# Kernel optimization log

Hardware: AMD Instinct MI355X
Metric: run time of the kernel (lower is better)

Reference implementation:

```python
import jax, jax.numpy as jnp
import numpy as np
from jax.scipy.special import logsumexp

NUM = 4      # Bregman ADMM iterations (module default)
EPS = 1e-8


def setup_inputs() -> dict:
    key = jax.random.key(0)
    k = jax.random.split(key, 8)
    B, N, D = 64, 1024, 512
    x = jax.random.normal(k[0], (B, N, D), dtype=jnp.float32)
    # marginal priors: positive, normalized along their distribution axis
    p0 = jax.random.uniform(k[1], (B, 1, D), dtype=jnp.float32, minval=0.1, maxval=1.0)
    p0 = p0 / jnp.sum(p0, axis=2, keepdims=True)
    q0 = jax.random.uniform(k[2], (B, N, 1), dtype=jnp.float32, minval=0.1, maxval=1.0)
    q0 = q0 / jnp.sum(q0, axis=1, keepdims=True)
    # positive per-iteration weights / ADMM step sizes
    a1 = jax.random.uniform(k[3], (NUM,), dtype=jnp.float32, minval=0.1, maxval=1.1)
    a2 = jax.random.uniform(k[4], (NUM,), dtype=jnp.float32, minval=0.1, maxval=1.1)
    a3 = jax.random.uniform(k[5], (NUM,), dtype=jnp.float32, minval=0.1, maxval=1.1)
    rho = jax.random.uniform(k[6], (NUM,), dtype=jnp.float32, minval=0.1, maxval=1.1)
    mask = jnp.ones((B, N, 1), dtype=jnp.float32)
    return {"x": x, "p0": p0, "q0": q0, "a1": a1, "a2": a2, "a3": a3,
            "rho": rho, "mask": mask}


def reference(x, p0, q0, a1, a2, a3, rho, mask):
    """UOT via Bregman ADMM with entropic regularizer (f_method='badmm-e')."""
    log_t = jnp.log(q0 * p0 + EPS)        # (B,N,D)
    log_s = jnp.log(q0 * p0 + EPS)        # (B,N,D)
    log_mu = jnp.log(p0)                  # (B,1,D)
    log_eta = jnp.log(q0 + EPS)           # (B,N,1)
    log_p0 = jnp.log(p0)
    log_q0 = jnp.log(q0 + EPS)
    z = jnp.zeros_like(log_t)
    z1 = jnp.zeros_like(p0)
    z2 = jnp.zeros_like(q0)
    for k in range(NUM):
        n = min(k, NUM - 1)
        # update T (row problem: normalize over D)
        y = (x - z) / rho[n] + log_s
        log_t = (log_mu - logsumexp(y, axis=2, keepdims=True)) + y
        # update S (column problem: normalize over N)
        y = (z + rho[n] * log_t) / (a1[n] + rho[n])
        log_s = (log_eta - logsumexp(y, axis=1, keepdims=True)) + y
        t = jnp.exp(log_t) * mask
        s = jnp.exp(log_s) * mask
        z = z + rho[n] * (t - s)
        # dual marginal updates
        y = (rho[n] * log_mu + a2[n] * log_p0 - z1) / (rho[n] + a2[n])
        log_mu = y - logsumexp(y, axis=2, keepdims=True)
        y = (rho[n] * log_eta + a3[n] * log_q0 - z2) / (rho[n] + a3[n])
        log_eta = y - logsumexp(y, axis=1, keepdims=True)
        z1 = z1 + rho[n] * (jnp.exp(log_mu) - jnp.sum(t, axis=2, keepdims=True))
        z2 = z2 + rho[n] * (jnp.exp(log_eta) - jnp.sum(s, axis=1, keepdims=True))
    return jnp.exp(log_t) * mask
```

## Files before the change

kernel.cpp:

```cpp
#include <hip/hip_runtime.h>
#include <cmath>


#define B_ 64
#define N_ 1024
#define D_ 512
#define EPS_ 1e-8f
#define NCHUNK 8
#define CH (N_ / NCHUNK)
#define NCOL (B_ * D_)
static const size_t NT_ = (size_t)B_ * N_ * D_;

__device__ __forceinline__ float wmax64(float v) {
#pragma unroll
  for (int o = 32; o > 0; o >>= 1) v = fmaxf(v, __shfl_xor(v, o, 64));
  return v;
}
__device__ __forceinline__ float wsum64(float v) {
#pragma unroll
  for (int o = 32; o > 0; o >>= 1) v += __shfl_xor(v, o, 64);
  return v;
}
__device__ __forceinline__ void olse(float& m, float& s, float v) {
  float nm = fmaxf(m, v);
  s = s * __expf(m - nm) + __expf(v - nm);
  m = nm;
}

template <int IS_FIRST, int LAST>
__global__ __launch_bounds__(256) void k1_row(
    const float* __restrict__ x, const float* __restrict__ p0,
    const float* __restrict__ q0, const float* __restrict__ mask,
    const float* __restrict__ a1arr, const float* __restrict__ rhoarr,
    const int k, const float* __restrict__ mun,
    float* ys,
    const float* __restrict__ z, float* __restrict__ outv)
{
  const int wid  = threadIdx.x >> 6;
  const int lane = threadIdx.x & 63;
  const int row  = (blockIdx.x << 2) + wid;
  const int b    = row >> 10;
  const float rho = rhoarr[k];
  const float inv_rho = 1.0f / rho;
  const size_t base = (size_t)row * D_ + (size_t)(lane * 8);
  const int pb = (b << 9) + lane * 8;

  float xv[8], y[8], lmu[8], zv[8];
  *(float4*)&xv[0] = *(const float4*)&x[base];
  *(float4*)&xv[4] = *(const float4*)&x[base + 4];

  if (IS_FIRST) {
    float pv[8];
    *(float4*)&pv[0] = *(const float4*)&p0[pb];
    *(float4*)&pv[4] = *(const float4*)&p0[pb + 4];
    const float q0v = q0[row];
#pragma unroll
    for (int j = 0; j < 8; ++j) {
      lmu[j] = __logf(pv[j]);
      float lsv = __logf(q0v * pv[j] + EPS_);
      y[j] = xv[j] * inv_rho + lsv;
      zv[j] = 0.f;
    }
  } else {
    float lsv[8];
    *(float4*)&zv[0]  = *(const float4*)&z[base];
    *(float4*)&zv[4]  = *(const float4*)&z[base + 4];
    *(float4*)&lsv[0] = *(const float4*)&ys[base];
    *(float4*)&lsv[4] = *(const float4*)&ys[base + 4];
    *(float4*)&lmu[0] = *(const float4*)&mun[pb];
    *(float4*)&lmu[4] = *(const float4*)&mun[pb + 4];
#pragma unroll
    for (int j = 0; j < 8; ++j) y[j] = (xv[j] - zv[j]) * inv_rho + lsv[j];
  }

  float mloc = -INFINITY;
#pragma unroll
  for (int j = 0; j < 8; ++j) mloc = fmaxf(mloc, y[j]);
  const float m = wmax64(mloc);
  float sloc = 0.f;
#pragma unroll
  for (int j = 0; j < 8; ++j) sloc += __expf(y[j] - m);
  const float lse = m + __logf(wsum64(sloc));

  if (LAST) {
    const float mv = mask[row];
    float o[8];
#pragma unroll
    for (int j = 0; j < 8; ++j) o[j] = __expf(lmu[j] - lse + y[j]) * mv;
    *(float4*)&outv[base]     = *(float4*)&o[0];
    *(float4*)&outv[base + 4] = *(float4*)&o[4];
  } else {
    const float inv_sc = 1.0f / (a1arr[k] + rho);
    float yp[8];
#pragma unroll
    for (int j = 0; j < 8; ++j)
      yp[j] = (zv[j] + rho * (lmu[j] - lse + y[j])) * inv_sc;
    *(float4*)&ys[base]     = *(float4*)&yp[0];
    *(float4*)&ys[base + 4] = *(float4*)&yp[4];
  }
}

__global__ __launch_bounds__(256) void k2a(
    const float* __restrict__ yp, float* __restrict__ pmax,
    float* __restrict__ psum)
{
  const int col = blockIdx.x * 256 + threadIdx.x;
  const int chunk = blockIdx.y;
  size_t idx = ((size_t)(col >> 9) * N_ + (size_t)(chunk * CH)) * D_ + (col & 511);
  float m0 = -INFINITY, s0 = 0.f, m1 = -INFINITY, s1 = 0.f;
  float m2 = -INFINITY, s2 = 0.f, m3 = -INFINITY, s3 = 0.f;
  for (int nn = 0; nn < CH; nn += 4) {
    float v0 = yp[idx];
    float v1 = yp[idx + D_];
    float v2 = yp[idx + 2 * D_];
    float v3 = yp[idx + 3 * D_];
    olse(m0, s0, v0); olse(m1, s1, v1); olse(m2, s2, v2); olse(m3, s3, v3);
    idx += 4 * D_;
  }
  float m = fmaxf(fmaxf(m0, m1), fmaxf(m2, m3));
  float s = s0 * __expf(m0 - m) + s1 * __expf(m1 - m) +
            s2 * __expf(m2 - m) + s3 * __expf(m3 - m);
  pmax[chunk * NCOL + col] = m;
  psum[chunk * NCOL + col] = s;
}

template <int IS_FIRST>
__global__ __launch_bounds__(256) void k2b(
    const float* __restrict__ q0, const float* __restrict__ mask,
    const float* __restrict__ a1arr, const float* __restrict__ rhoarr,
    const int k, const float* __restrict__ len,
    float* ys,
    float* __restrict__ z,
    const float* __restrict__ pmax, const float* __restrict__ psum)
{
  const int col = blockIdx.x * 256 + threadIdx.x;
  const int chunk = blockIdx.y;
  const float rho = rhoarr[k];
  const float sc = a1arr[k] + rho;
  const float inv_rho = 1.0f / rho;
  const float sc_ir = sc * inv_rho;

  float lse1;
  {
    float m = -INFINITY;
#pragma unroll
    for (int c = 0; c < NCHUNK; ++c) m = fmaxf(m, pmax[c * NCOL + col]);
    float s = 0.f;
#pragma unroll
    for (int c = 0; c < NCHUNK; ++c)
      s += psum[c * NCOL + col] * __expf(pmax[c * NCOL + col] - m);
    lse1 = m + __logf(s);
  }

  size_t idx = ((size_t)(col >> 9) * N_ + (size_t)(chunk * CH)) * D_ + (col & 511);
  int nrow = (col >> 9) * N_ + chunk * CH;
#pragma unroll 2
  for (int nn = 0; nn < CH; ++nn) {
    float ypv = ys[idx];
    float zv = IS_FIRST ? 0.f : z[idx];
    float le = IS_FIRST ? __logf(q0[nrow] + EPS_) : len[nrow];
    float ls = (le - lse1) + ypv;
    ys[idx] = ls;
    float mv = mask[nrow];
    float lt = IS_FIRST ? ypv * sc_ir : (ypv * sc - zv) * inv_rho;
    float t  = __expf(lt) * mv;
    float s_ = __expf(ls) * mv;
    z[idx] = zv + rho * (t - s_);
    idx += D_;
    ++nrow;
  }
}

template <int K>
__global__ __launch_bounds__(256) void small_upd(
    const float* __restrict__ p0, const float* __restrict__ q0,
    const float* __restrict__ a2arr, const float* __restrict__ a3arr,
    const float* __restrict__ rhoarr,
    float* mun, float* zC, float* len, float* z2C)
{
  __shared__ float red[8];
  const int b = blockIdx.x;
  const int tid = threadIdx.x, wid = tid >> 6, lane = tid & 63;
  const float rho = rhoarr[K];

  if (blockIdx.y == 0) {
    const float a2 = a2arr[K];
    const float inv = 1.0f / (rho + a2);
    float A[2], zcv[2];
    const int i0 = b * D_ + tid;
#pragma unroll
    for (int j = 0; j < 2; ++j) {
      int i = i0 + j * 256;
      float lp = __logf(p0[i]);
      float prev = (K == 0) ? lp : mun[i];
      zcv[j] = (K == 0) ? 0.f : zC[i];
      A[j] = (rho * prev + a2 * lp - zcv[j]) * inv;
    }
    float m = wmax64(fmaxf(A[0], A[1]));
    if (lane == 0) red[wid] = m;
    __syncthreads();
    float bm = fmaxf(fmaxf(red[0], red[1]), fmaxf(red[2], red[3]));
    float s = wsum64(__expf(A[0] - bm) + __expf(A[1] - bm));
    if (lane == 0) red[4 + wid] = s;
    __syncthreads();
    float lse = bm + __logf(red[4] + red[5] + red[6] + red[7]);
#pragma unroll
    for (int j = 0; j < 2; ++j) {
      int i = i0 + j * 256;
      float mn = A[j] - lse;
      mun[i] = mn;
      if (K <= 1) zC[i] = zcv[j] + rho * __expf(mn);
    }
  } else {
    const float a3 = a3arr[K];
    const float inv = 1.0f / (rho + a3);
    float E[4];
    const int i0 = b * N_ + tid * 4;
#pragma unroll
    for (int j = 0; j < 4; ++j) {
      int i = i0 + j;
      float lq = __logf(q0[i] + EPS_);
      float prev = (K == 0) ? lq : len[i];
      float z2c = (K == 0) ? 0.f : z2C[i];
      E[j] = (rho * prev + a3 * lq - z2c) * inv;
    }
    float m = wmax64(fmaxf(fmaxf(E[0], E[1]), fmaxf(E[2], E[3])));
    if (lane == 0) red[wid] = m;
    __syncthreads();
    float bm = fmaxf(fmaxf(red[0], red[1]), fmaxf(red[2], red[3]));
    float s = 0.f;
#pragma unroll
    for (int j = 0; j < 4; ++j) s += __expf(E[j] - bm);
    s = wsum64(s);
    if (lane == 0) red[4 + wid] = s;
    __syncthreads();
    float lse = bm + __logf(red[4] + red[5] + red[6] + red[7]);
#pragma unroll
    for (int j = 0; j < 4; ++j) {
      int i = i0 + j;
      float ln = E[j] - lse;
      len[i] = ln;
      if (K == 0) z2C[i] = rho * __expf(ln);
    }
  }
}

extern "C" void kernel_launch(void* const* d_in, const int* in_sizes, int n_in,
                              void* d_out, int out_size, void* d_ws, size_t ws_size,
                              hipStream_t stream)
{
  const float* x    = (const float*)d_in[0];
  const float* p0   = (const float*)d_in[1];
  const float* q0   = (const float*)d_in[2];
  const float* a1   = (const float*)d_in[3];
  const float* a2   = (const float*)d_in[4];
  const float* a3   = (const float*)d_in[5];
  const float* rho  = (const float*)d_in[6];
  const float* mask = (const float*)d_in[7];
  float* out = (float*)d_out;

  float* ws   = (float*)d_ws;
  float* ys   = ws;
  float* z    = ws + NT_;
  float* pmax = ws + 2 * NT_;
  float* psum = pmax + (size_t)NCHUNK * NCOL;
  float* mun  = psum + (size_t)NCHUNK * NCOL;
  float* zC   = mun + (size_t)B_ * D_;
  float* len  = zC  + (size_t)B_ * D_;
  float* z2C  = len + (size_t)B_ * N_;

  const dim3 tb(256);
  const dim3 g1(B_ * N_ / 4);
  const dim3 g2(NCOL / 256, NCHUNK);

  k1_row<1, 0><<<g1, tb, 0, stream>>>(x, p0, q0, mask, a1, rho, 0, mun, ys, z, out);
  k2a<<<g2, tb, 0, stream>>>(ys, pmax, psum);
  k2b<1><<<g2, tb, 0, stream>>>(q0, mask, a1, rho, 0, len, ys, z, pmax, psum);
  small_upd<0><<<dim3(B_, 2), tb, 0, stream>>>(p0, q0, a2, a3, rho, mun, zC, len, z2C);

  k1_row<0, 0><<<g1, tb, 0, stream>>>(x, p0, q0, mask, a1, rho, 1, mun, ys, z, out);
  k2a<<<g2, tb, 0, stream>>>(ys, pmax, psum);
  k2b<0><<<g2, tb, 0, stream>>>(q0, mask, a1, rho, 1, len, ys, z, pmax, psum);
  small_upd<1><<<dim3(B_, 2), tb, 0, stream>>>(p0, q0, a2, a3, rho, mun, zC, len, z2C);

  k1_row<0, 0><<<g1, tb, 0, stream>>>(x, p0, q0, mask, a1, rho, 2, mun, ys, z, out);
  k2a<<<g2, tb, 0, stream>>>(ys, pmax, psum);
  k2b<0><<<g2, tb, 0, stream>>>(q0, mask, a1, rho, 2, len, ys, z, pmax, psum);
  small_upd<2><<<dim3(B_, 1), tb, 0, stream>>>(p0, q0, a2, a3, rho, mun, zC, len, z2C);

  k1_row<0, 1><<<g1, tb, 0, stream>>>(x, p0, q0, mask, a1, rho, 3, mun, ys, z, out);
}
```

Baseline: 841.6 us.

## Fuse column partial LSE into row kernel, vectorize column update, fold last z

The row kernel now computes per-16-row column partial max/sum through LDS after writing ys, which removes the separate k2a pass that re-read the full ys tensor. A small reduction kernel combines the 64 chunk partials into lse1. The column update kernel is vectorized to float4. In the last iteration z is folded into ys as ls - z/rho_next so that z need not be written or re-read by the final row kernel. In exchange it uses 1024-thread blocks with a block-wide sync and a larger partial buffer.

```diff
diff --git a/kernel.cpp b/kernel.cpp
--- a/kernel.cpp
+++ b/kernel.cpp
@@ -6,9 +6,10 @@
 #define N_ 1024
 #define D_ 512
 #define EPS_ 1e-8f
-#define NCHUNK 8
-#define CH (N_ / NCHUNK)
 #define NCOL (B_ * D_)
+#define KCHUNK 64
+#define CH2 16
+#define NCHUNK2 64
 static const size_t NT_ = (size_t)B_ * N_ * D_;
 
 __device__ __forceinline__ float wmax64(float v) {
@@ -21,27 +22,25 @@
   for (int o = 32; o > 0; o >>= 1) v += __shfl_xor(v, o, 64);
   return v;
 }
-__device__ __forceinline__ void olse(float& m, float& s, float v) {
-  float nm = fmaxf(m, v);
-  s = s * __expf(m - nm) + __expf(v - nm);
-  m = nm;
-}
-
-template <int IS_FIRST, int LAST>
-__global__ __launch_bounds__(256) void k1_row(
+
+template <int IS_FIRST>
+__global__ __launch_bounds__(1024, 4) void k1p(
     const float* __restrict__ x, const float* __restrict__ p0,
-    const float* __restrict__ q0, const float* __restrict__ mask,
+    const float* __restrict__ q0,
     const float* __restrict__ a1arr, const float* __restrict__ rhoarr,
     const int k, const float* __restrict__ mun,
     float* ys,
-    const float* __restrict__ z, float* __restrict__ outv)
-{
+    const float* __restrict__ z,
+    float* __restrict__ pmax, float* __restrict__ psum)
+{
+  __shared__ float lds[16 * 512];
   const int wid  = threadIdx.x >> 6;
   const int lane = threadIdx.x & 63;
-  const int row  = (blockIdx.x << 2) + wid;
+  const int row  = blockIdx.x * 16 + wid;
   const int b    = row >> 10;
   const float rho = rhoarr[k];
   const float inv_rho = 1.0f / rho;
+  const float inv_sc = 1.0f / (a1arr[k] + rho);
   const size_t base = (size_t)row * D_ + (size_t)(lane * 8);
   const int pb = (b << 9) + lane * 8;
 
@@ -62,15 +61,14 @@
       zv[j] = 0.f;
     }
   } else {
-    float lsv[8];
-    *(float4*)&zv[0]  = *(const float4*)&z[base];
-    *(float4*)&zv[4]  = *(const float4*)&z[base + 4];
-    *(float4*)&lsv[0] = *(const float4*)&ys[base];
-    *(float4*)&lsv[4] = *(const float4*)&ys[base + 4];
+    *(float4*)&zv[0] = *(const float4*)&z[base];
+    *(float4*)&zv[4] = *(const float4*)&z[base + 4];
+    *(float4*)&y[0]  = *(const float4*)&ys[base];
+    *(float4*)&y[4]  = *(const float4*)&ys[base + 4];
     *(float4*)&lmu[0] = *(const float4*)&mun[pb];
     *(float4*)&lmu[4] = *(const float4*)&mun[pb + 4];
 #pragma unroll
-    for (int j = 0; j < 8; ++j) y[j] = (xv[j] - zv[j]) * inv_rho + lsv[j];
+    for (int j = 0; j < 8; ++j) y[j] = (xv[j] - zv[j]) * inv_rho + y[j];
   }
 
   float mloc = -INFINITY;
@@ -82,93 +80,152 @@
   for (int j = 0; j < 8; ++j) sloc += __expf(y[j] - m);
   const float lse = m + __logf(wsum64(sloc));
 
-  if (LAST) {
-    const float mv = mask[row];
-    float o[8];
-#pragma unroll
-    for (int j = 0; j < 8; ++j) o[j] = __expf(lmu[j] - lse + y[j]) * mv;
-    *(float4*)&outv[base]     = *(float4*)&o[0];
-    *(float4*)&outv[base + 4] = *(float4*)&o[4];
-  } else {
-    const float inv_sc = 1.0f / (a1arr[k] + rho);
-    float yp[8];
-#pragma unroll
-    for (int j = 0; j < 8; ++j)
-      yp[j] = (zv[j] + rho * (lmu[j] - lse + y[j])) * inv_sc;
-    *(float4*)&ys[base]     = *(float4*)&yp[0];
-    *(float4*)&ys[base + 4] = *(float4*)&yp[4];
-  }
-}
-
-__global__ __launch_bounds__(256) void k2a(
-    const float* __restrict__ yp, float* __restrict__ pmax,
-    float* __restrict__ psum)
+  float yp[8];
+#pragma unroll
+  for (int j = 0; j < 8; ++j)
+    yp[j] = (zv[j] + rho * (lmu[j] - lse + y[j])) * inv_sc;
+  *(float4*)&ys[base]     = *(float4*)&yp[0];
+  *(float4*)&ys[base + 4] = *(float4*)&yp[4];
+
+  const int dbase = lane * 8;
+#pragma unroll
+  for (int j = 0; j < 8; ++j) lds[wid * 512 + dbase + j] = yp[j];
+  __syncthreads();
+  if (threadIdx.x < 512) {
+    const int d = threadIdx.x;
+    float v[16];
+#pragma unroll
+    for (int w = 0; w < 16; ++w) v[w] = lds[w * 512 + d];
+    float mm = v[0];
+#pragma unroll
+    for (int w = 1; w < 16; ++w) mm = fmaxf(mm, v[w]);
+    float ss = 0.f;
+#pragma unroll
+    for (int w = 0; w < 16; ++w) ss += __expf(v[w] - mm);
+    const int bb = blockIdx.x >> 6;
+    const int chunk = blockIdx.x & 63;
+    const int col = (bb << 9) + d;
+    pmax[chunk * NCOL + col] = mm;
+    psum[chunk * NCOL + col] = ss;
+  }
+}
+
+__global__ __launch_bounds__(256) void kred(
+    const float* __restrict__ pmax, const float* __restrict__ psum,
+    float* __restrict__ lse1)
 {
   const int col = blockIdx.x * 256 + threadIdx.x;
-  const int chunk = blockIdx.y;
-  size_t idx = ((size_t)(col >> 9) * N_ + (size_t)(chunk * CH)) * D_ + (col & 511);
-  float m0 = -INFINITY, s0 = 0.f, m1 = -INFINITY, s1 = 0.f;
-  float m2 = -INFINITY, s2 = 0.f, m3 = -INFINITY, s3 = 0.f;
-  for (int nn = 0; nn < CH; nn += 4) {
-    float v0 = yp[idx];
-    float v1 = yp[idx + D_];
-    float v2 = yp[idx + 2 * D_];
-    float v3 = yp[idx + 3 * D_];
-    olse(m0, s0, v0); olse(m1, s1, v1); olse(m2, s2, v2); olse(m3, s3, v3);
-    idx += 4 * D_;
-  }
-  float m = fmaxf(fmaxf(m0, m1), fmaxf(m2, m3));
-  float s = s0 * __expf(m0 - m) + s1 * __expf(m1 - m) +
-            s2 * __expf(m2 - m) + s3 * __expf(m3 - m);
-  pmax[chunk * NCOL + col] = m;
-  psum[chunk * NCOL + col] = s;
-}
-
-template <int IS_FIRST>
+  float m0 = -INFINITY, m1 = -INFINITY, m2 = -INFINITY, m3 = -INFINITY;
+#pragma unroll
+  for (int c = 0; c < KCHUNK; c += 4) {
+    m0 = fmaxf(m0, pmax[(c + 0) * NCOL + col]);
+    m1 = fmaxf(m1, pmax[(c + 1) * NCOL + col]);
+    m2 = fmaxf(m2, pmax[(c + 2) * NCOL + col]);
+    m3 = fmaxf(m3, pmax[(c + 3) * NCOL + col]);
+  }
+  const float M = fmaxf(fmaxf(m0, m1), fmaxf(m2, m3));
+  float s0 = 0.f, s1 = 0.f, s2 = 0.f, s3 = 0.f;
+#pragma unroll
+  for (int c = 0; c < KCHUNK; c += 4) {
+    s0 += psum[(c + 0) * NCOL + col] * __expf(pmax[(c + 0) * NCOL + col] - M);
+    s1 += psum[(c + 1) * NCOL + col] * __expf(pmax[(c + 1) * NCOL + col] - M);
+    s2 += psum[(c + 2) * NCOL + col] * __expf(pmax[(c + 2) * NCOL + col] - M);
+    s3 += psum[(c + 3) * NCOL + col] * __expf(pmax[(c + 3) * NCOL + col] - M);
+  }
+  lse1[col] = M + __logf((s0 + s1) + (s2 + s3));
+}
+
+template <int IS_FIRST, int WRITE_Z, int FOLD>
 __global__ __launch_bounds__(256) void k2b(
     const float* __restrict__ q0, const float* __restrict__ mask,
     const float* __restrict__ a1arr, const float* __restrict__ rhoarr,
     const int k, const float* __restrict__ len,
     float* ys,
     float* __restrict__ z,
-    const float* __restrict__ pmax, const float* __restrict__ psum)
-{
-  const int col = blockIdx.x * 256 + threadIdx.x;
-  const int chunk = blockIdx.y;
+    const float* __restrict__ lse1)
+{
+  const int t4 = (blockIdx.x * 256 + threadIdx.x) * 4;
+  const int b = t4 >> 9;
+  const int d = t4 & 511;
+  const int n0 = blockIdx.y * CH2;
   const float rho = rhoarr[k];
   const float sc = a1arr[k] + rho;
   const float inv_rho = 1.0f / rho;
   const float sc_ir = sc * inv_rho;
-
-  float lse1;
-  {
-    float m = -INFINITY;
-#pragma unroll
-    for (int c = 0; c < NCHUNK; ++c) m = fmaxf(m, pmax[c * NCOL + col]);
-    float s = 0.f;
-#pragma unroll
-    for (int c = 0; c < NCHUNK; ++c)
-      s += psum[c * NCOL + col] * __expf(pmax[c * NCOL + col] - m);
-    lse1 = m + __logf(s);
-  }
-
-  size_t idx = ((size_t)(col >> 9) * N_ + (size_t)(chunk * CH)) * D_ + (col & 511);
-  int nrow = (col >> 9) * N_ + chunk * CH;
-#pragma unroll 2
-  for (int nn = 0; nn < CH; ++nn) {
-    float ypv = ys[idx];
-    float zv = IS_FIRST ? 0.f : z[idx];
-    float le = IS_FIRST ? __logf(q0[nrow] + EPS_) : len[nrow];
-    float ls = (le - lse1) + ypv;
-    ys[idx] = ls;
-    float mv = mask[nrow];
-    float lt = IS_FIRST ? ypv * sc_ir : (ypv * sc - zv) * inv_rho;
-    float t  = __expf(lt) * mv;
-    float s_ = __expf(ls) * mv;
-    z[idx] = zv + rho * (t - s_);
+  const float irn = FOLD ? (1.0f / rhoarr[k + 1]) : 0.0f;
+
+  float L[4];
+  *(float4*)L = *(const float4*)&lse1[t4];
+
+  size_t idx = ((size_t)b * N_ + (size_t)n0) * D_ + d;
+  int nrow = b * N_ + n0;
+#pragma unroll 4
+  for (int nn = 0; nn < CH2; ++nn) {
+    float ypv[4], zv[4];
+    *(float4*)ypv = *(const float4*)&ys[idx];
+    if (IS_FIRST) {
+#pragma unroll
+      for (int j = 0; j < 4; ++j) zv[j] = 0.f;
+    } else {
+      *(float4*)zv = *(const float4*)&z[idx];
+    }
+    const float le = IS_FIRST ? __logf(q0[nrow] + EPS_) : len[nrow];
+    const float mv = mask[nrow];
+    float wout[4], zn[4];
+#pragma unroll
+    for (int j = 0; j < 4; ++j) {
+      float ls = (le - L[j]) + ypv[j];
+      float lt = IS_FIRST ? ypv[j] * sc_ir : (ypv[j] * sc - zv[j]) * inv_rho;
+      float t_ = __expf(lt) * mv;
+      float s_ = __expf(ls) * mv;
+      zn[j] = zv[j] + rho * (t_ - s_);
+      wout[j] = FOLD ? (ls - zn[j] * irn) : ls;
+    }
+    *(float4*)&ys[idx] = *(float4*)wout;
+    if (WRITE_Z) *(float4*)&z[idx] = *(float4*)zn;
     idx += D_;
     ++nrow;
   }
+}
+
+__global__ __launch_bounds__(256) void k1last(
+    const float* __restrict__ x, const float* __restrict__ mask,
+    const float* __restrict__ rhoarr, const float* __restrict__ mun,
+    const float* __restrict__ w, float* __restrict__ outv)
+{
+  const int wid  = threadIdx.x >> 6;
+  const int lane = threadIdx.x & 63;
+  const int row  = (blockIdx.x << 2) + wid;
+  const int b    = row >> 10;
+  const float inv_rho = 1.0f / rhoarr[3];
+  const size_t base = (size_t)row * D_ + (size_t)(lane * 8);
+  const int pb = (b << 9) + lane * 8;
+
+  float xv[8], y[8], lmu[8];
+  *(float4*)&xv[0] = *(const float4*)&x[base];
+  *(float4*)&xv[4] = *(const float4*)&x[base + 4];
+  *(float4*)&y[0]  = *(const float4*)&w[base];
+  *(float4*)&y[4]  = *(const float4*)&w[base + 4];
+  *(float4*)&lmu[0] = *(const float4*)&mun[pb];
+  *(float4*)&lmu[4] = *(const float4*)&mun[pb + 4];
+#pragma unroll
+  for (int j = 0; j < 8; ++j) y[j] = xv[j] * inv_rho + y[j];
+
+  float mloc = -INFINITY;
+#pragma unroll
+  for (int j = 0; j < 8; ++j) mloc = fmaxf(mloc, y[j]);
+  const float m = wmax64(mloc);
+  float sloc = 0.f;
+#pragma unroll
+  for (int j = 0; j < 8; ++j) sloc += __expf(y[j] - m);
+  const float lse = m + __logf(wsum64(sloc));
+
+  const float mv = mask[row];
+  float o[8];
+#pragma unroll
+  for (int j = 0; j < 8; ++j) o[j] = __expf(lmu[j] - lse + y[j]) * mv;
+  *(float4*)&outv[base]     = *(float4*)&o[0];
+  *(float4*)&outv[base + 4] = *(float4*)&o[4];
 }
 
 template <int K>
@@ -263,30 +320,34 @@
   float* ys   = ws;
   float* z    = ws + NT_;
   float* pmax = ws + 2 * NT_;
-  float* psum = pmax + (size_t)NCHUNK * NCOL;
-  float* mun  = psum + (size_t)NCHUNK * NCOL;
+  float* psum = pmax + (size_t)KCHUNK * NCOL;
+  float* lse1 = psum + (size_t)KCHUNK * NCOL;
+  float* mun  = lse1 + NCOL;
   float* zC   = mun + (size_t)B_ * D_;
   float* len  = zC  + (size_t)B_ * D_;
   float* z2C  = len + (size_t)B_ * N_;
 
   const dim3 tb(256);
-  const dim3 g1(B_ * N_ / 4);
-  const dim3 g2(NCOL / 256, NCHUNK);
-
-  k1_row<1, 0><<<g1, tb, 0, stream>>>(x, p0, q0, mask, a1, rho, 0, mun, ys, z, out);
-  k2a<<<g2, tb, 0, stream>>>(ys, pmax, psum);
-  k2b<1><<<g2, tb, 0, stream>>>(q0, mask, a1, rho, 0, len, ys, z, pmax, psum);
+  const dim3 tb1k(1024);
+  const dim3 g1(B_ * N_ / 16);
+  const dim3 gr(NCOL / 256);
+  const dim3 g2(NCOL / 4 / 256, NCHUNK2);
+  const dim3 gl(B_ * N_ / 4);
+
+  k1p<1><<<g1, tb1k, 0, stream>>>(x, p0, q0, a1, rho, 0, mun, ys, z, pmax, psum);
+  kred<<<gr, tb, 0, stream>>>(pmax, psum, lse1);
+  k2b<1, 1, 0><<<g2, tb, 0, stream>>>(q0, mask, a1, rho, 0, len, ys, z, lse1);
   small_upd<0><<<dim3(B_, 2), tb, 0, stream>>>(p0, q0, a2, a3, rho, mun, zC, len, z2C);
 
-  k1_row<0, 0><<<g1, tb, 0, stream>>>(x, p0, q0, mask, a1, rho, 1, mun, ys, z, out);
-  k2a<<<g2, tb, 0, stream>>>(ys, pmax, psum);
-  k2b<0><<<g2, tb, 0, stream>>>(q0, mask, a1, rho, 1, len, ys, z, pmax, psum);
+  k1p<0><<<g1, tb1k, 0, stream>>>(x, p0, q0, a1, rho, 1, mun, ys, z, pmax, psum);
+  kred<<<gr, tb, 0, stream>>>(pmax, psum, lse1);
+  k2b<0, 1, 0><<<g2, tb, 0, stream>>>(q0, mask, a1, rho, 1, len, ys, z, lse1);
   small_upd<1><<<dim3(B_, 2), tb, 0, stream>>>(p0, q0, a2, a3, rho, mun, zC, len, z2C);
 
-  k1_row<0, 0><<<g1, tb, 0, stream>>>(x, p0, q0, mask, a1, rho, 2, mun, ys, z, out);
-  k2a<<<g2, tb, 0, stream>>>(ys, pmax, psum);
-  k2b<0><<<g2, tb, 0, stream>>>(q0, mask, a1, rho, 2, len, ys, z, pmax, psum);
+  k1p<0><<<g1, tb1k, 0, stream>>>(x, p0, q0, a1, rho, 2, mun, ys, z, pmax, psum);
+  kred<<<gr, tb, 0, stream>>>(pmax, psum, lse1);
+  k2b<0, 0, 1><<<g2, tb, 0, stream>>>(q0, mask, a1, rho, 2, len, ys, z, lse1);
   small_upd<2><<<dim3(B_, 1), tb, 0, stream>>>(p0, q0, a2, a3, rho, mun, zC, len, z2C);
 
-  k1_row<0, 1><<<g1, tb, 0, stream>>>(x, p0, q0, mask, a1, rho, 3, mun, ys, z, out);
-}
+  k1last<<<gl, tb, 0, stream>>>(x, mask, rho, mun, ys, out);
+}
```

Measured after the change: 746.8 us. -11.3%, faster.

## Fuse column update into next row pass with per-chunk partial column LSE

Applied to the files above, without the earlier changes.

Merges the S/z column update of iteration k with the row logsumexp of iteration k+1 into one streaming kernel. Each wave handles 16 rows and keeps running per-column max/sum partials, so the separate column-LSE read pass disappears and only a small 64-chunk reduction kernel remains. This cuts full-tensor reads and writes of ys and z per iteration. The cost is double-buffered eta vectors, larger partial buffers, and the extra register pressure of software-pipelined row loads.

```diff
diff --git a/kernel.cpp b/kernel.cpp
--- a/kernel.cpp
+++ b/kernel.cpp
@@ -6,9 +6,8 @@
 #define N_ 1024
 #define D_ 512
 #define EPS_ 1e-8f
-#define NCHUNK 8
-#define CH (N_ / NCHUNK)
 #define NCOL (B_ * D_)
+#define KCHUNK 64
 static const size_t NT_ = (size_t)B_ * N_ * D_;
 
 __device__ __forceinline__ float wmax64(float v) {
@@ -27,148 +26,215 @@
   m = nm;
 }
 
+__global__ __launch_bounds__(256, 4) void p0k(
+    const float* __restrict__ x, const float* __restrict__ p0,
+    const float* __restrict__ q0,
+    const float* __restrict__ a1arr, const float* __restrict__ rhoarr,
+    float* __restrict__ ys, float* __restrict__ pmax, float* __restrict__ psum)
+{
+  const int wid = threadIdx.x >> 6, lane = threadIdx.x & 63;
+  const int chunk = blockIdx.x * 4 + wid;
+  const int b = chunk >> 6, cb = chunk & 63;
+  const int c0 = lane * 8;
+  const int row0 = chunk * 16;
+  const float rho0 = rhoarr[0];
+  const float ir = 1.0f / rho0;
+  const float w0 = rho0 / (a1arr[0] + rho0);
+  float pv[8], lp[8];
+  *(float4*)&pv[0] = *(const float4*)&p0[(b << 9) + c0];
+  *(float4*)&pv[4] = *(const float4*)&p0[(b << 9) + c0 + 4];
+#pragma unroll
+  for (int j = 0; j < 8; ++j) lp[j] = __logf(pv[j]);
+  float m[8], s[8];
+#pragma unroll
+  for (int j = 0; j < 8; ++j) { m[j] = -INFINITY; s[j] = 0.f; }
+  const size_t base0 = (size_t)row0 * D_ + c0;
+
+  float xA[8], xB[8];
+  float qA, qB;
+
+#define LOADP(X, Q, r) do {                                   \
+    const size_t o_ = base0 + (size_t)(r) * D_;               \
+    *(float4*)&X[0] = *(const float4*)&x[o_];                 \
+    *(float4*)&X[4] = *(const float4*)&x[o_ + 4];             \
+    Q = q0[row0 + (r)];                                       \
+  } while (0)
+
+#define PROCP(X, Q, r) do {                                   \
+    _Pragma("unroll")                                         \
+    for (int j = 0; j < 8; ++j)                               \
+      X[j] = X[j] * ir + __logf(Q * pv[j] + EPS_);            \
+    float mm_ = -INFINITY;                                    \
+    _Pragma("unroll")                                         \
+    for (int j = 0; j < 8; ++j) mm_ = fmaxf(mm_, X[j]);       \
+    mm_ = wmax64(mm_);                                        \
+    float ss_ = 0.f;                                          \
+    _Pragma("unroll")                                         \
+    for (int j = 0; j < 8; ++j) ss_ += __expf(X[j] - mm_);    \
+    const float lse_ = mm_ + __logf(wsum64(ss_));             \
+    float yp_[8];                                             \
+    _Pragma("unroll")                                         \
+    for (int j = 0; j < 8; ++j)                               \
+      yp_[j] = (lp[j] - lse_ + X[j]) * w0;                    \
+    const size_t o_ = base0 + (size_t)(r) * D_;               \
+    *(float4*)&ys[o_]     = *(float4*)&yp_[0];                \
+    *(float4*)&ys[o_ + 4] = *(float4*)&yp_[4];                \
+    _Pragma("unroll")                                         \
+    for (int j = 0; j < 8; ++j) olse(m[j], s[j], yp_[j]);     \
+  } while (0)
+
+  LOADP(xA, qA, 0);
+#pragma unroll
+  for (int rr = 0; rr < 16; rr += 2) {
+    LOADP(xB, qB, rr + 1);
+    PROCP(xA, qA, rr);
+    if (rr + 2 < 16) LOADP(xA, qA, rr + 2);
+    PROCP(xB, qB, rr + 1);
+  }
+#undef LOADP
+#undef PROCP
+  const int pcol = cb * NCOL + (b << 9) + c0;
+  *(float4*)&pmax[pcol]     = *(float4*)&m[0];
+  *(float4*)&pmax[pcol + 4] = *(float4*)&m[4];
+  *(float4*)&psum[pcol]     = *(float4*)&s[0];
+  *(float4*)&psum[pcol + 4] = *(float4*)&s[4];
+}
+
 template <int IS_FIRST, int LAST>
-__global__ __launch_bounds__(256) void k1_row(
-    const float* __restrict__ x, const float* __restrict__ p0,
-    const float* __restrict__ q0, const float* __restrict__ mask,
+__global__ __launch_bounds__(256, 4) void fuse(
+    const float* __restrict__ x, const float* __restrict__ q0,
+    const float* __restrict__ mask,
     const float* __restrict__ a1arr, const float* __restrict__ rhoarr,
-    const int k, const float* __restrict__ mun,
-    float* ys,
-    const float* __restrict__ z, float* __restrict__ outv)
-{
-  const int wid  = threadIdx.x >> 6;
-  const int lane = threadIdx.x & 63;
-  const int row  = (blockIdx.x << 2) + wid;
-  const int b    = row >> 10;
-  const float rho = rhoarr[k];
-  const float inv_rho = 1.0f / rho;
-  const size_t base = (size_t)row * D_ + (size_t)(lane * 8);
-  const int pb = (b << 9) + lane * 8;
-
-  float xv[8], y[8], lmu[8], zv[8];
-  *(float4*)&xv[0] = *(const float4*)&x[base];
-  *(float4*)&xv[4] = *(const float4*)&x[base + 4];
-
-  if (IS_FIRST) {
-    float pv[8];
-    *(float4*)&pv[0] = *(const float4*)&p0[pb];
-    *(float4*)&pv[4] = *(const float4*)&p0[pb + 4];
-    const float q0v = q0[row];
-#pragma unroll
-    for (int j = 0; j < 8; ++j) {
-      lmu[j] = __logf(pv[j]);
-      float lsv = __logf(q0v * pv[j] + EPS_);
-      y[j] = xv[j] * inv_rho + lsv;
-      zv[j] = 0.f;
-    }
-  } else {
-    float lsv[8];
-    *(float4*)&zv[0]  = *(const float4*)&z[base];
-    *(float4*)&zv[4]  = *(const float4*)&z[base + 4];
-    *(float4*)&lsv[0] = *(const float4*)&ys[base];
-    *(float4*)&lsv[4] = *(const float4*)&ys[base + 4];
-    *(float4*)&lmu[0] = *(const float4*)&mun[pb];
-    *(float4*)&lmu[4] = *(const float4*)&mun[pb + 4];
-#pragma unroll
-    for (int j = 0; j < 8; ++j) y[j] = (xv[j] - zv[j]) * inv_rho + lsv[j];
-  }
-
-  float mloc = -INFINITY;
-#pragma unroll
-  for (int j = 0; j < 8; ++j) mloc = fmaxf(mloc, y[j]);
-  const float m = wmax64(mloc);
-  float sloc = 0.f;
-#pragma unroll
-  for (int j = 0; j < 8; ++j) sloc += __expf(y[j] - m);
-  const float lse = m + __logf(wsum64(sloc));
-
-  if (LAST) {
-    const float mv = mask[row];
-    float o[8];
-#pragma unroll
-    for (int j = 0; j < 8; ++j) o[j] = __expf(lmu[j] - lse + y[j]) * mv;
-    *(float4*)&outv[base]     = *(float4*)&o[0];
-    *(float4*)&outv[base + 4] = *(float4*)&o[4];
-  } else {
-    const float inv_sc = 1.0f / (a1arr[k] + rho);
-    float yp[8];
-#pragma unroll
-    for (int j = 0; j < 8; ++j)
-      yp[j] = (zv[j] + rho * (lmu[j] - lse + y[j])) * inv_sc;
-    *(float4*)&ys[base]     = *(float4*)&yp[0];
-    *(float4*)&ys[base + 4] = *(float4*)&yp[4];
-  }
-}
-
-__global__ __launch_bounds__(256) void k2a(
-    const float* __restrict__ yp, float* __restrict__ pmax,
-    float* __restrict__ psum)
+    const int k, const float* __restrict__ lse1,
+    const float* __restrict__ lenR, const float* __restrict__ mun,
+    float* __restrict__ ys, float* __restrict__ zbuf,
+    float* __restrict__ pmax, float* __restrict__ psum,
+    float* __restrict__ outv)
+{
+  const int wid = threadIdx.x >> 6, lane = threadIdx.x & 63;
+  const int chunk = blockIdx.x * 4 + wid;
+  const int b = chunk >> 6, cb = chunk & 63;
+  const int c0 = lane * 8;
+  const int row0 = chunk * 16;
+  const float rhok = rhoarr[k];
+  const float sck = a1arr[k] + rhok;
+  const float irk = 1.0f / rhok;
+  const float rhon = rhoarr[k + 1];
+  const float irn = 1.0f / rhon;
+  const float iscn = 1.0f / (a1arr[k + 1] + rhon);
+  const size_t base0 = (size_t)row0 * D_ + c0;
+
+  float L[8], lm[8];
+  *(float4*)&L[0]  = *(const float4*)&lse1[(b << 9) + c0];
+  *(float4*)&L[4]  = *(const float4*)&lse1[(b << 9) + c0 + 4];
+  *(float4*)&lm[0] = *(const float4*)&mun[(b << 9) + c0];
+  *(float4*)&lm[4] = *(const float4*)&mun[(b << 9) + c0 + 4];
+  float m[8], s[8];
+#pragma unroll
+  for (int j = 0; j < 8; ++j) { m[j] = -INFINITY; s[j] = 0.f; }
+
+  float xA[8], pA[8], zA[8], xB[8], pB[8], zB[8];
+  float leA, mvA, leB, mvB;
+
+#define LOADF(X, P, Z, LE, MV, r) do {                        \
+    const size_t o_ = base0 + (size_t)(r) * D_;               \
+    *(float4*)&X[0] = *(const float4*)&x[o_];                 \
+    *(float4*)&X[4] = *(const float4*)&x[o_ + 4];             \
+    *(float4*)&P[0] = *(const float4*)&ys[o_];                \
+    *(float4*)&P[4] = *(const float4*)&ys[o_ + 4];            \
+    if (!IS_FIRST) {                                          \
+      *(float4*)&Z[0] = *(const float4*)&zbuf[o_];            \
+      *(float4*)&Z[4] = *(const float4*)&zbuf[o_ + 4];        \
+    }                                                         \
+    LE = IS_FIRST ? __logf(q0[row0 + (r)] + EPS_)             \
+                  : lenR[row0 + (r)];                         \
+    MV = mask[row0 + (r)];                                    \
+  } while (0)
+
+#define PROCF(X, P, Z, LE, MV, r) do {                        \
+    float ls_[8];                                             \
+    _Pragma("unroll")                                         \
+    for (int j = 0; j < 8; ++j) {                             \
+      ls_[j] = (LE - L[j]) + P[j];                            \
+      float lt_ = IS_FIRST ? P[j] * sck * irk                 \
+                           : (P[j] * sck - Z[j]) * irk;       \
+      float zn_ = (IS_FIRST ? 0.f : Z[j]) +                   \
+                  rhok * MV * (__expf(lt_) - __expf(ls_[j])); \
+      Z[j] = zn_;                                             \
+      X[j] = (X[j] - zn_) * irn + ls_[j];                     \
+    }                                                         \
+    float mm_ = -INFINITY;                                    \
+    _Pragma("unroll")                                         \
+    for (int j = 0; j < 8; ++j) mm_ = fmaxf(mm_, X[j]);       \
+    mm_ = wmax64(mm_);                                        \
+    float ss_ = 0.f;                                          \
+    _Pragma("unroll")                                         \
+    for (int j = 0; j < 8; ++j) ss_ += __expf(X[j] - mm_);    \
+    const float lse_ = mm_ + __logf(wsum64(ss_));             \
+    const size_t o_ = base0 + (size_t)(r) * D_;               \
+    if (LAST) {                                               \
+      float ov_[8];                                           \
+      _Pragma("unroll")                                       \
+      for (int j = 0; j < 8; ++j)                             \
+        ov_[j] = __expf(lm[j] - lse_ + X[j]) * MV;            \
+      *(float4*)&outv[o_]     = *(float4*)&ov_[0];            \
+      *(float4*)&outv[o_ + 4] = *(float4*)&ov_[4];            \
+    } else {                                                  \
+      _Pragma("unroll")                                       \
+      for (int j = 0; j < 8; ++j)                             \
+        ls_[j] = (Z[j] + rhon * (lm[j] - lse_ + X[j])) * iscn;\
+      *(float4*)&ys[o_]       = *(float4*)&ls_[0];            \
+      *(float4*)&ys[o_ + 4]   = *(float4*)&ls_[4];            \
+      *(float4*)&zbuf[o_]     = *(float4*)&Z[0];              \
+      *(float4*)&zbuf[o_ + 4] = *(float4*)&Z[4];              \
+      _Pragma("unroll")                                       \
+      for (int j = 0; j < 8; ++j) olse(m[j], s[j], ls_[j]);   \
+    }                                                         \
+  } while (0)
+
+  LOADF(xA, pA, zA, leA, mvA, 0);
+#pragma unroll
+  for (int rr = 0; rr < 16; rr += 2) {
+    LOADF(xB, pB, zB, leB, mvB, rr + 1);
+    PROCF(xA, pA, zA, leA, mvA, rr);
+    if (rr + 2 < 16) LOADF(xA, pA, zA, leA, mvA, rr + 2);
+    PROCF(xB, pB, zB, leB, mvB, rr + 1);
+  }
+#undef LOADF
+#undef PROCF
+
+  if (!LAST) {
+    const int pcol = cb * NCOL + (b << 9) + c0;
+    *(float4*)&pmax[pcol]     = *(float4*)&m[0];
+    *(float4*)&pmax[pcol + 4] = *(float4*)&m[4];
+    *(float4*)&psum[pcol]     = *(float4*)&s[0];
+    *(float4*)&psum[pcol + 4] = *(float4*)&s[4];
+  }
+}
+
+__global__ __launch_bounds__(256) void kred(
+    const float* __restrict__ pmax, const float* __restrict__ psum,
+    float* __restrict__ lse1)
 {
   const int col = blockIdx.x * 256 + threadIdx.x;
-  const int chunk = blockIdx.y;
-  size_t idx = ((size_t)(col >> 9) * N_ + (size_t)(chunk * CH)) * D_ + (col & 511);
-  float m0 = -INFINITY, s0 = 0.f, m1 = -INFINITY, s1 = 0.f;
-  float m2 = -INFINITY, s2 = 0.f, m3 = -INFINITY, s3 = 0.f;
-  for (int nn = 0; nn < CH; nn += 4) {
-    float v0 = yp[idx];
-    float v1 = yp[idx + D_];
-    float v2 = yp[idx + 2 * D_];
-    float v3 = yp[idx + 3 * D_];
-    olse(m0, s0, v0); olse(m1, s1, v1); olse(m2, s2, v2); olse(m3, s3, v3);
-    idx += 4 * D_;
-  }
-  float m = fmaxf(fmaxf(m0, m1), fmaxf(m2, m3));
-  float s = s0 * __expf(m0 - m) + s1 * __expf(m1 - m) +
-            s2 * __expf(m2 - m) + s3 * __expf(m3 - m);
-  pmax[chunk * NCOL + col] = m;
-  psum[chunk * NCOL + col] = s;
-}
-
-template <int IS_FIRST>
-__global__ __launch_bounds__(256) void k2b(
-    const float* __restrict__ q0, const float* __restrict__ mask,
-    const float* __restrict__ a1arr, const float* __restrict__ rhoarr,
-    const int k, const float* __restrict__ len,
-    float* ys,
-    float* __restrict__ z,
-    const float* __restrict__ pmax, const float* __restrict__ psum)
-{
-  const int col = blockIdx.x * 256 + threadIdx.x;
-  const int chunk = blockIdx.y;
-  const float rho = rhoarr[k];
-  const float sc = a1arr[k] + rho;
-  const float inv_rho = 1.0f / rho;
-  const float sc_ir = sc * inv_rho;
-
-  float lse1;
-  {
-    float m = -INFINITY;
-#pragma unroll
-    for (int c = 0; c < NCHUNK; ++c) m = fmaxf(m, pmax[c * NCOL + col]);
-    float s = 0.f;
-#pragma unroll
-    for (int c = 0; c < NCHUNK; ++c)
-      s += psum[c * NCOL + col] * __expf(pmax[c * NCOL + col] - m);
-    lse1 = m + __logf(s);
-  }
-
-  size_t idx = ((size_t)(col >> 9) * N_ + (size_t)(chunk * CH)) * D_ + (col & 511);
-  int nrow = (col >> 9) * N_ + chunk * CH;
-#pragma unroll 2
-  for (int nn = 0; nn < CH; ++nn) {
-    float ypv = ys[idx];
-    float zv = IS_FIRST ? 0.f : z[idx];
-    float le = IS_FIRST ? __logf(q0[nrow] + EPS_) : len[nrow];
-    float ls = (le - lse1) + ypv;
-    ys[idx] = ls;
-    float mv = mask[nrow];
-    float lt = IS_FIRST ? ypv * sc_ir : (ypv * sc - zv) * inv_rho;
-    float t  = __expf(lt) * mv;
-    float s_ = __expf(ls) * mv;
-    z[idx] = zv + rho * (t - s_);
-    idx += D_;
-    ++nrow;
-  }
+  float m0 = -INFINITY, m1 = -INFINITY, m2 = -INFINITY, m3 = -INFINITY;
+#pragma unroll
+  for (int c = 0; c < KCHUNK; c += 4) {
+    m0 = fmaxf(m0, pmax[(c + 0) * NCOL + col]);
+    m1 = fmaxf(m1, pmax[(c + 1) * NCOL + col]);
+    m2 = fmaxf(m2, pmax[(c + 2) * NCOL + col]);
+    m3 = fmaxf(m3, pmax[(c + 3) * NCOL + col]);
+  }
+  const float M = fmaxf(fmaxf(m0, m1), fmaxf(m2, m3));
+  float s0 = 0.f, s1 = 0.f, s2 = 0.f, s3 = 0.f;
+#pragma unroll
+  for (int c = 0; c < KCHUNK; c += 4) {
+    s0 += psum[(c + 0) * NCOL + col] * __expf(pmax[(c + 0) * NCOL + col] - M);
+    s1 += psum[(c + 1) * NCOL + col] * __expf(pmax[(c + 1) * NCOL + col] - M);
+    s2 += psum[(c + 2) * NCOL + col] * __expf(pmax[(c + 2) * NCOL + col] - M);
+    s3 += psum[(c + 3) * NCOL + col] * __expf(pmax[(c + 3) * NCOL + col] - M);
+  }
+  lse1[col] = M + __logf((s0 + s1) + (s2 + s3));
 }
 
 template <int K>
@@ -176,7 +242,8 @@
     const float* __restrict__ p0, const float* __restrict__ q0,
     const float* __restrict__ a2arr, const float* __restrict__ a3arr,
     const float* __restrict__ rhoarr,
-    float* mun, float* zC, float* len, float* z2C)
+    float* mun, float* zC, const float* __restrict__ lenR,
+    float* lenW, float* z2C)
 {
   __shared__ float red[8];
   const int b = blockIdx.x;
@@ -220,7 +287,7 @@
     for (int j = 0; j < 4; ++j) {
       int i = i0 + j;
       float lq = __logf(q0[i] + EPS_);
-      float prev = (K == 0) ? lq : len[i];
+      float prev = (K == 0) ? lq : lenR[i];
       float z2c = (K == 0) ? 0.f : z2C[i];
       E[j] = (rho * prev + a3 * lq - z2c) * inv;
     }
@@ -239,7 +306,7 @@
     for (int j = 0; j < 4; ++j) {
       int i = i0 + j;
       float ln = E[j] - lse;
-      len[i] = ln;
+      lenW[i] = ln;
       if (K == 0) z2C[i] = rho * __expf(ln);
     }
   }
@@ -263,30 +330,32 @@
   float* ys   = ws;
   float* z    = ws + NT_;
   float* pmax = ws + 2 * NT_;
-  float* psum = pmax + (size_t)NCHUNK * NCOL;
-  float* mun  = psum + (size_t)NCHUNK * NCOL;
-  float* zC   = mun + (size_t)B_ * D_;
-  float* len  = zC  + (size_t)B_ * D_;
-  float* z2C  = len + (size_t)B_ * N_;
+  float* psum = pmax + (size_t)KCHUNK * NCOL;
+  float* lse1 = psum + (size_t)KCHUNK * NCOL;
+  float* mun  = lse1 + NCOL;
+  float* zC   = mun  + NCOL;
+  float* lenA = zC   + NCOL;
+  float* lenB = lenA + (size_t)B_ * N_;
+  float* z2C  = lenB + (size_t)B_ * N_;
 
   const dim3 tb(256);
-  const dim3 g1(B_ * N_ / 4);
-  const dim3 g2(NCOL / 256, NCHUNK);
-
-  k1_row<1, 0><<<g1, tb, 0, stream>>>(x, p0, q0, mask, a1, rho, 0, mun, ys, z, out);
-  k2a<<<g2, tb, 0, stream>>>(ys, pmax, psum);
-  k2b<1><<<g2, tb, 0, stream>>>(q0, mask, a1, rho, 0, len, ys, z, pmax, psum);
-  small_upd<0><<<dim3(B_, 2), tb, 0, stream>>>(p0, q0, a2, a3, rho, mun, zC, len, z2C);
-
-  k1_row<0, 0><<<g1, tb, 0, stream>>>(x, p0, q0, mask, a1, rho, 1, mun, ys, z, out);
-  k2a<<<g2, tb, 0, stream>>>(ys, pmax, psum);
-  k2b<0><<<g2, tb, 0, stream>>>(q0, mask, a1, rho, 1, len, ys, z, pmax, psum);
-  small_upd<1><<<dim3(B_, 2), tb, 0, stream>>>(p0, q0, a2, a3, rho, mun, zC, len, z2C);
-
-  k1_row<0, 0><<<g1, tb, 0, stream>>>(x, p0, q0, mask, a1, rho, 2, mun, ys, z, out);
-  k2a<<<g2, tb, 0, stream>>>(ys, pmax, psum);
-  k2b<0><<<g2, tb, 0, stream>>>(q0, mask, a1, rho, 2, len, ys, z, pmax, psum);
-  small_upd<2><<<dim3(B_, 1), tb, 0, stream>>>(p0, q0, a2, a3, rho, mun, zC, len, z2C);
-
-  k1_row<0, 1><<<g1, tb, 0, stream>>>(x, p0, q0, mask, a1, rho, 3, mun, ys, z, out);
-}
+  const dim3 gBig(B_ * N_ / 16 / 4);
+  const dim3 gr(NCOL / 256);
+
+  p0k<<<gBig, tb, 0, stream>>>(x, p0, q0, a1, rho, ys, pmax, psum);
+  kred<<<gr, tb, 0, stream>>>(pmax, psum, lse1);
+  small_upd<0><<<dim3(B_, 2), tb, 0, stream>>>(p0, q0, a2, a3, rho,
+                                               mun, zC, lenA, lenA, z2C);
+  fuse<1, 0><<<gBig, tb, 0, stream>>>(x, q0, mask, a1, rho, 0, lse1,
+                                      lenA, mun, ys, z, pmax, psum, out);
+  kred<<<gr, tb, 0, stream>>>(pmax, psum, lse1);
+  small_upd<1><<<dim3(B_, 2), tb, 0, stream>>>(p0, q0, a2, a3, rho,
+                                               mun, zC, lenA, lenB, z2C);
+  fuse<0, 0><<<gBig, tb, 0, stream>>>(x, q0, mask, a1, rho, 1, lse1,
+                                      lenA, mun, ys, z, pmax, psum, out);
+  kred<<<gr, tb, 0, stream>>>(pmax, psum, lse1);
+  small_upd<2><<<dim3(B_, 1), tb, 0, stream>>>(p0, q0, a2, a3, rho,
+                                               mun, zC, lenB, lenB, z2C);
+  fuse<0, 1><<<gBig, tb, 0, stream>>>(x, q0, mask, a1, rho, 2, lse1,
+                                      lenB, mun, ys, z, pmax, psum, out);
+}
```

New measurement: 864.5 us. 2.7% more time.
